# Kernel optimization log

Hardware: AMD Instinct MI355X
Metric: run time of the kernel (lower is better)

The kernel has to match this reference:

```python
import jax, jax.numpy as jnp
import numpy as np

N = 1_000_000          # number of points
V = 65536              # number of voxels / groups (static stand-in for unique(coors))
IN_CH = 64             # 3 xyz + 61 extra features
HID = 64               # feat_channels = [64, 64]
REL_HID = 16           # rel_mlp_hidden_dims = [16]
XYZ_NORM = jnp.asarray([1.0, 1.0, 1.0], dtype=jnp.float32)
REL_DIST_SCALER = jnp.float32(1.0)


def setup_inputs() -> dict:
    key = jax.random.key(0)
    ks = jax.random.split(key, 10)

    def lin(k, i, o):
        return (jax.random.normal(k, (i, o), jnp.float32) / np.sqrt(i)).astype(jnp.float32)

    return {
        "points_xyzs": jax.random.normal(ks[0], (N, 3), jnp.float32),
        "points_feat": jax.random.normal(ks[1], (N, IN_CH - 3), jnp.float32),
        "f_cluster": jax.random.normal(ks[2], (N, 3), jnp.float32),
        "coors": jax.random.randint(ks[3], (N,), 0, V, jnp.int32),
        # rel_mlp: Linear(3,16)+BN+ReLU, Linear(16,64)+BN+ReLU (inference BN folded to scale/shift)
        "rel_w0": lin(ks[4], 3, REL_HID),
        "rel_g0": jnp.ones((REL_HID,), jnp.float32),
        "rel_b0": jnp.zeros((REL_HID,), jnp.float32),
        "rel_w1": lin(ks[5], REL_HID, IN_CH),
        "rel_g1": jnp.ones((IN_CH,), jnp.float32),
        "rel_b1": jnp.zeros((IN_CH,), jnp.float32),
        # vfe layer 0: Linear(64,64)+BN+ReLU;  vfe layer 1: Linear(128,64)+BN+ReLU (in_filters*=2 for i>0)
        "vfe_w0": lin(ks[6], IN_CH, HID),
        "vfe_g0": jnp.ones((HID,), jnp.float32),
        "vfe_b0": jnp.zeros((HID,), jnp.float32),
        "vfe_w1": lin(ks[7], 2 * HID, HID),
        "vfe_g1": jnp.ones((HID,), jnp.float32),
        "vfe_b1": jnp.zeros((HID,), jnp.float32),
    }


def _bn_relu(x, g, b):
    # inference BatchNorm1d folded into per-channel scale/shift, then ReLU
    return jax.nn.relu(x * g + b)


def _forward(points_xyzs, points_feat, f_cluster, coors,
             rel_w0, rel_g0, rel_b0, rel_w1, rel_g1, rel_b1,
             vfe_w0, vfe_g0, vfe_b0, vfe_w1, vfe_g1, vfe_b1):
    xyz = points_xyzs / XYZ_NORM                              # [N, 3]
    feats = jnp.concatenate([xyz, points_feat], axis=-1)      # [N, IN_CH]
    shortcut = feats
    fc = f_cluster / REL_DIST_SCALER                          # [N, 3]
    # relative-position MLP gating: features *= rel_mlp(f_cluster)
    h = _bn_relu(fc @ rel_w0, rel_g0, rel_b0)                 # [N, REL_HID]
    gate = _bn_relu(h @ rel_w1, rel_g1, rel_b1)               # [N, IN_CH]
    feats = feats * gate
    # VFE layer 0: per-point MLP -> voxel-wise scatter max -> gather back -> concat
    p0 = _bn_relu(feats @ vfe_w0, vfe_g0, vfe_b0)             # [N, HID]
    v0 = jax.ops.segment_max(p0, coors, num_segments=V)       # [V, HID]
    v0 = jnp.where(jnp.isfinite(v0), v0, jnp.float32(0.0))    # empty voxels -> 0
    feats = jnp.concatenate([p0, v0[coors]], axis=-1)         # [N, 2*HID]
    # VFE layer 1 (last): per-point MLP, plus residual shortcut (shapes match)
    p1 = _bn_relu(feats @ vfe_w1, vfe_g1, vfe_b1)             # [N, HID]
    return p1 + shortcut


def reference(points_xyzs, points_feat, f_cluster, coors,
              rel_w0, rel_g0, rel_b0, rel_w1, rel_g1, rel_b1,
              vfe_w0, vfe_g0, vfe_b0, vfe_w1, vfe_g1, vfe_b1):
    return _forward(points_xyzs, points_feat, f_cluster, coors,
                    rel_w0, rel_g0, rel_b0, rel_w1, rel_g1, rel_b1,
                    vfe_w0, vfe_g0, vfe_b0, vfe_w1, vfe_g1, vfe_b1)
```

## Files before the change

kernel.cpp:

```cpp
#include <hip/hip_runtime.h>


#define VVOX 65536

__global__ void __launch_bounds__(256)
sir_k1a(const float* __restrict__ xyz,
        const float* __restrict__ pfeat,
        const float* __restrict__ fclu,
        const float* __restrict__ rw0,
        const float* __restrict__ rg0,
        const float* __restrict__ rb0,
        const float* __restrict__ rw1,
        const float* __restrict__ rg1,
        const float* __restrict__ rb1,
        float* __restrict__ G,
        int npts)
{
    __shared__ float s_w0[48];
    __shared__ float s_b0[16];
    __shared__ float s_w1t[1024];
    __shared__ float s_b1[64];

    const int t = threadIdx.x;
    if (t < 48) s_w0[t] = rw0[t] * rg0[t & 15];
    if (t < 16) s_b0[t] = rb0[t];
    for (int i = t; i < 1024; i += 256) {
        int k = i >> 4, j = i & 15;
        s_w1t[i] = rw1[j * 64 + k] * rg1[k];
    }
    if (t < 64) s_b1[t] = rb1[t];
    __syncthreads();

    const int pt = blockIdx.x * 256 + t;
    if (pt >= npts) return;

    const float* cr = fclu + (size_t)pt * 3;
    const float c0 = cr[0], c1 = cr[1], c2 = cr[2];
    float h[16];
    #pragma unroll
    for (int j = 0; j < 16; ++j) {
        float v = s_b0[j];
        v = fmaf(c0, s_w0[j], v);
        v = fmaf(c1, s_w0[16 + j], v);
        v = fmaf(c2, s_w0[32 + j], v);
        h[j] = fmaxf(v, 0.f);
    }

    const float* xr = xyz + (size_t)pt * 3;
    const float* fr = pfeat + (size_t)pt * 61;
    float4* Grow = reinterpret_cast<float4*>(G + (size_t)pt * 64);

    #pragma unroll 4
    for (int k4 = 0; k4 < 16; ++k4) {
        float u[4];
        #pragma unroll
        for (int kk = 0; kk < 4; ++kk) {
            const int k = k4 * 4 + kk;
            const float* w1k = s_w1t + k * 16;
            float g0 = s_b1[k], g1 = 0.f, g2 = 0.f, g3 = 0.f;
            #pragma unroll
            for (int j = 0; j < 4; ++j) {
                g0 = fmaf(h[j],      w1k[j],      g0);
                g1 = fmaf(h[4 + j],  w1k[4 + j],  g1);
                g2 = fmaf(h[8 + j],  w1k[8 + j],  g2);
                g3 = fmaf(h[12 + j], w1k[12 + j], g3);
            }
            const float g = fmaxf((g0 + g1) + (g2 + g3), 0.f);
            const float fk = (k < 3) ? xr[k] : fr[k - 3];
            u[kk] = fk * g;
        }
        float4 uu;
        uu.x = u[0]; uu.y = u[1]; uu.z = u[2]; uu.w = u[3];
        Grow[k4] = uu;
    }
}

__global__ void __launch_bounds__(256)
sir_k1b(const float* __restrict__ G,
        const int* __restrict__ coors,
        const float* __restrict__ vw0,
        const float* __restrict__ vg0,
        const float* __restrict__ vb0,
        unsigned int* __restrict__ vmax,
        float* __restrict__ p0out,
        int npts)
{
    __shared__ float s_w[4096];
    __shared__ float s_b[64];
    const int t = threadIdx.x;
    for (int i = t; i < 4096; i += 256) s_w[i] = vw0[i] * vg0[i & 63];
    if (t < 64) s_b[t] = vb0[t];
    __syncthreads();

    const int cg = t & 3;
    const int ps = t >> 2;
    const int base = blockIdx.x * 256;

    int p[4]; bool ok[4];
    const float4* Gp[4];
    #pragma unroll
    for (int i = 0; i < 4; ++i) {
        p[i] = base + ps + 64 * i;
        ok[i] = p[i] < npts;
        const int pc = ok[i] ? p[i] : 0;
        Gp[i] = reinterpret_cast<const float4*>(G + (size_t)pc * 64);
    }

    float acc[4][16];
    #pragma unroll
    for (int i = 0; i < 4; ++i)
        #pragma unroll
        for (int c = 0; c < 16; ++c) acc[i][c] = s_b[cg * 16 + c];

    float4 gv[4], gvn[4];
    #pragma unroll
    for (int i = 0; i < 4; ++i) gv[i] = Gp[i][0];

    for (int k4 = 0; k4 < 16; ++k4) {
        const int k4n = (k4 + 1) & 15;
        #pragma unroll
        for (int i = 0; i < 4; ++i) gvn[i] = Gp[i][k4n];
        const float* wb = s_w + k4 * 256 + cg * 16;
        #pragma unroll
        for (int kk = 0; kk < 4; ++kk) {
            const float* wr = wb + kk * 64;
            #pragma unroll
            for (int i = 0; i < 4; ++i) {
                const float ga[4] = { gv[i].x, gv[i].y, gv[i].z, gv[i].w };
                const float gk = ga[kk];
                #pragma unroll
                for (int c = 0; c < 16; ++c)
                    acc[i][c] = fmaf(gk, wr[c], acc[i][c]);
            }
        }
        #pragma unroll
        for (int i = 0; i < 4; ++i) gv[i] = gvn[i];
    }

    __syncthreads();

    #pragma unroll
    for (int i = 0; i < 4; ++i) {
        if (!ok[i]) continue;
        const int vox = coors[p[i]];
        unsigned int* vrow = vmax + (size_t)vox * 64 + cg * 16;
        const uint4* vrow4 = reinterpret_cast<const uint4*>(vrow);
        float4* orow = reinterpret_cast<float4*>(p0out + (size_t)p[i] * 64 + cg * 16);
        #pragma unroll
        for (int q = 0; q < 4; ++q) {
            const uint4 cur = vrow4[q];
            float4 u;
            u.x = fmaxf(acc[i][q * 4 + 0], 0.f);
            u.y = fmaxf(acc[i][q * 4 + 1], 0.f);
            u.z = fmaxf(acc[i][q * 4 + 2], 0.f);
            u.w = fmaxf(acc[i][q * 4 + 3], 0.f);
            orow[q] = u;
            if (__float_as_uint(u.x) > cur.x) atomicMax(vrow + q * 4 + 0, __float_as_uint(u.x));
            if (__float_as_uint(u.y) > cur.y) atomicMax(vrow + q * 4 + 1, __float_as_uint(u.y));
            if (__float_as_uint(u.z) > cur.z) atomicMax(vrow + q * 4 + 2, __float_as_uint(u.z));
            if (__float_as_uint(u.w) > cur.w) atomicMax(vrow + q * 4 + 3, __float_as_uint(u.w));
        }
    }
}

__global__ void __launch_bounds__(256)
sir_k2(const float* __restrict__ xyz,
       const float* __restrict__ pfeat,
       const int* __restrict__ coors,
       const float* __restrict__ vw1,
       const float* __restrict__ vg1,
       const float* __restrict__ vb1,
       const float* __restrict__ vmaxf,
       float* __restrict__ io,
       int npts)
{
    __shared__ float s_w[8192];
    __shared__ float s_b[64];
    const int t = threadIdx.x;
    for (int i = t; i < 8192; i += 256) s_w[i] = vw1[i] * vg1[i & 63];
    if (t < 64) s_b[t] = vb1[t];
    __syncthreads();

    const int cg = t & 3;
    const int ps = t >> 2;
    const int base = blockIdx.x * 256;

    int p[4]; bool ok[4];
    const float4* prow[4];
    const float4* vrow[4];
    #pragma unroll
    for (int i = 0; i < 4; ++i) {
        p[i] = base + ps + 64 * i;
        ok[i] = p[i] < npts;
        const int pc = ok[i] ? p[i] : 0;
        prow[i] = reinterpret_cast<const float4*>(io + (size_t)pc * 64);
        const int vox = coors[pc];
        vrow[i] = reinterpret_cast<const float4*>(vmaxf + (size_t)vox * 64);
    }

    float acc[4][16];
    #pragma unroll
    for (int i = 0; i < 4; ++i)
        #pragma unroll
        for (int c = 0; c < 16; ++c) acc[i][c] = s_b[cg * 16 + c];

    float4 gv[4], gvn[4];

    #pragma unroll
    for (int i = 0; i < 4; ++i) gv[i] = prow[i][0];
    for (int k4 = 0; k4 < 16; ++k4) {
        const int k4n = (k4 + 1) & 15;
        #pragma unroll
        for (int i = 0; i < 4; ++i) gvn[i] = prow[i][k4n];
        const float* wb = s_w + k4 * 256 + cg * 16;
        #pragma unroll
        for (int kk = 0; kk < 4; ++kk) {
            const float* wr = wb + kk * 64;
            #pragma unroll
            for (int i = 0; i < 4; ++i) {
                const float ga[4] = { gv[i].x, gv[i].y, gv[i].z, gv[i].w };
                const float gk = ga[kk];
                #pragma unroll
                for (int c = 0; c < 16; ++c)
                    acc[i][c] = fmaf(gk, wr[c], acc[i][c]);
            }
        }
        #pragma unroll
        for (int i = 0; i < 4; ++i) gv[i] = gvn[i];
    }

    #pragma unroll
    for (int i = 0; i < 4; ++i) gv[i] = vrow[i][0];
    for (int k4 = 0; k4 < 16; ++k4) {
        const int k4n = (k4 + 1) & 15;
        #pragma unroll
        for (int i = 0; i < 4; ++i) gvn[i] = vrow[i][k4n];
        const float* wb = s_w + 4096 + k4 * 256 + cg * 16;
        #pragma unroll
        for (int kk = 0; kk < 4; ++kk) {
            const float* wr = wb + kk * 64;
            #pragma unroll
            for (int i = 0; i < 4; ++i) {
                const float ga[4] = { gv[i].x, gv[i].y, gv[i].z, gv[i].w };
                const float gk = ga[kk];
                #pragma unroll
                for (int c = 0; c < 16; ++c)
                    acc[i][c] = fmaf(gk, wr[c], acc[i][c]);
            }
        }
        #pragma unroll
        for (int i = 0; i < 4; ++i) gv[i] = gvn[i];
    }

    __syncthreads();

    #pragma unroll
    for (int i = 0; i < 4; ++i) {
        if (!ok[i]) continue;
        const float* xr = xyz + (size_t)p[i] * 3;
        const float* fr = pfeat + (size_t)p[i] * 61;
        float4* orow = reinterpret_cast<float4*>(io + (size_t)p[i] * 64 + cg * 16);
        #pragma unroll
        for (int q = 0; q < 4; ++q) {
            const int c = cg * 16 + q * 4;
            const float s0 = (c + 0 < 3) ? xr[c + 0] : fr[c - 3];
            const float s1 = (c + 1 < 3) ? xr[c + 1] : fr[c - 2];
            const float s2 = (c + 2 < 3) ? xr[c + 2] : fr[c - 1];
            const float s3 = (c + 3 < 3) ? xr[c + 3] : fr[c + 0];
            float4 u;
            u.x = fmaxf(acc[i][q * 4 + 0], 0.f) + s0;
            u.y = fmaxf(acc[i][q * 4 + 1], 0.f) + s1;
            u.z = fmaxf(acc[i][q * 4 + 2], 0.f) + s2;
            u.w = fmaxf(acc[i][q * 4 + 3], 0.f) + s3;
            orow[q] = u;
        }
    }
}

extern "C" void kernel_launch(void* const* d_in, const int* in_sizes, int n_in,
                              void* d_out, int out_size, void* d_ws, size_t ws_size,
                              hipStream_t stream) {
    const float* xyz   = (const float*)d_in[0];
    const float* pfeat = (const float*)d_in[1];
    const float* fclu  = (const float*)d_in[2];
    const int*   coors = (const int*)d_in[3];
    const float* rw0 = (const float*)d_in[4];
    const float* rg0 = (const float*)d_in[5];
    const float* rb0 = (const float*)d_in[6];
    const float* rw1 = (const float*)d_in[7];
    const float* rg1 = (const float*)d_in[8];
    const float* rb1 = (const float*)d_in[9];
    const float* vw0 = (const float*)d_in[10];
    const float* vg0 = (const float*)d_in[11];
    const float* vb0 = (const float*)d_in[12];
    const float* vw1 = (const float*)d_in[13];
    const float* vg1 = (const float*)d_in[14];
    const float* vb1 = (const float*)d_in[15];

    float*        out  = (float*)d_out;
    unsigned int* vmax = (unsigned int*)d_ws;
    const int npts = in_sizes[3];
    const int blocks = (npts + 255) / 256;

    hipMemsetAsync(d_ws, 0, (size_t)VVOX * 64 * sizeof(float), stream);

    hipLaunchKernelGGL(sir_k1a, dim3(blocks), dim3(256), 0, stream,
                       xyz, pfeat, fclu,
                       rw0, rg0, rb0, rw1, rg1, rb1,
                       out, npts);

    hipLaunchKernelGGL(sir_k1b, dim3(blocks), dim3(256), 0, stream,
                       out, coors, vw0, vg0, vb0, vmax, out, npts);

    hipLaunchKernelGGL(sir_k2, dim3(blocks), dim3(256), 0, stream,
                       xyz, pfeat, coors,
                       vw1, vg1, vb1, (const float*)d_ws, out, npts);
}
```

Measured before the change: 1.945 ms.

## Sort points by voxel via counting sort and fuse gate MLP into VFE0

Adds a histogram, single-block scan and permutation pass that build a voxel-sorted point order. A separate pass then does the scatter-max in sorted order, and the second VFE layer also runs in sorted order, so voxel-max rows and atomics stay local. The rel-MLP gating and the first VFE matmul are fused into one per-point kernel with 64 accumulators per thread, which removes the intermediate G buffer round trip. The cost is extra sort kernels with contended atomics, a serial scan, gathered row reads of p0 in sorted order, and possibly high register pressure. An unsorted fallback is kept for when the workspace is too small.

```diff
diff --git a/kernel.cpp b/kernel.cpp
--- a/kernel.cpp
+++ b/kernel.cpp
@@ -4,22 +4,73 @@
 #define VVOX 65536
 
 __global__ void __launch_bounds__(256)
-sir_k1a(const float* __restrict__ xyz,
-        const float* __restrict__ pfeat,
-        const float* __restrict__ fclu,
-        const float* __restrict__ rw0,
-        const float* __restrict__ rg0,
-        const float* __restrict__ rb0,
-        const float* __restrict__ rw1,
-        const float* __restrict__ rg1,
-        const float* __restrict__ rb1,
-        float* __restrict__ G,
-        int npts)
+sir_hist(const int* __restrict__ coors, unsigned int* __restrict__ cnt, int npts)
+{
+    const int p = blockIdx.x * 256 + threadIdx.x;
+    if (p < npts) atomicAdd(&cnt[coors[p]], 1u);
+}
+
+__global__ void __launch_bounds__(1024)
+sir_scan(unsigned int* __restrict__ cnt)
+{
+    __shared__ unsigned int s[1024];
+    const int t = threadIdx.x;
+    unsigned int sum = 0;
+    for (int i = 0; i < 64; ++i) sum += cnt[t * 64 + i];
+    s[t] = sum;
+    __syncthreads();
+    for (int off = 1; off < 1024; off <<= 1) {
+        unsigned int v = (t >= off) ? s[t - off] : 0u;
+        __syncthreads();
+        s[t] += v;
+        __syncthreads();
+    }
+    unsigned int run = s[t] - sum;
+    for (int i = 0; i < 64; ++i) {
+        const unsigned int c = cnt[t * 64 + i];
+        cnt[t * 64 + i] = run;
+        run += c;
+    }
+}
+
+__global__ void __launch_bounds__(256)
+sir_permute(const int* __restrict__ coors, unsigned int* __restrict__ cursor,
+            unsigned int* __restrict__ perm, unsigned int* __restrict__ voxs,
+            int npts)
+{
+    const int p = blockIdx.x * 256 + threadIdx.x;
+    if (p >= npts) return;
+    const int vox = coors[p];
+    const unsigned int j = atomicAdd(&cursor[vox], 1u);
+    perm[j] = (unsigned int)p;
+    voxs[j] = (unsigned int)vox;
+}
+
+template <bool SCATTER>
+__global__ void __launch_bounds__(256)
+sir_k1(const float* __restrict__ xyz,
+       const float* __restrict__ pfeat,
+       const float* __restrict__ fclu,
+       const int* __restrict__ coors,
+       const float* __restrict__ rw0,
+       const float* __restrict__ rg0,
+       const float* __restrict__ rb0,
+       const float* __restrict__ rw1,
+       const float* __restrict__ rg1,
+       const float* __restrict__ rb1,
+       const float* __restrict__ vw0,
+       const float* __restrict__ vg0,
+       const float* __restrict__ vb0,
+       unsigned int* __restrict__ vmax,
+       float* __restrict__ p0out,
+       int npts)
 {
     __shared__ float s_w0[48];
     __shared__ float s_b0[16];
     __shared__ float s_w1t[1024];
     __shared__ float s_b1[64];
+    __shared__ float s_vw0[4096];
+    __shared__ float s_vb0[64];
 
     const int t = threadIdx.x;
     if (t < 48) s_w0[t] = rw0[t] * rg0[t & 15];
@@ -29,6 +80,8 @@
         s_w1t[i] = rw1[j * 64 + k] * rg1[k];
     }
     if (t < 64) s_b1[t] = rb1[t];
+    for (int i = t; i < 4096; i += 256) s_vw0[i] = vw0[i] * vg0[i & 63];
+    if (t < 64) s_vb0[t] = vb0[t];
     __syncthreads();
 
     const int pt = blockIdx.x * 256 + t;
@@ -46,127 +99,94 @@
         h[j] = fmaxf(v, 0.f);
     }
 
+    float acc[64];
+    #pragma unroll
+    for (int c = 0; c < 64; ++c) acc[c] = s_vb0[c];
+
     const float* xr = xyz + (size_t)pt * 3;
     const float* fr = pfeat + (size_t)pt * 61;
-    float4* Grow = reinterpret_cast<float4*>(G + (size_t)pt * 64);
-
-    #pragma unroll 4
-    for (int k4 = 0; k4 < 16; ++k4) {
-        float u[4];
-        #pragma unroll
-        for (int kk = 0; kk < 4; ++kk) {
-            const int k = k4 * 4 + kk;
-            const float* w1k = s_w1t + k * 16;
-            float g0 = s_b1[k], g1 = 0.f, g2 = 0.f, g3 = 0.f;
-            #pragma unroll
-            for (int j = 0; j < 4; ++j) {
-                g0 = fmaf(h[j],      w1k[j],      g0);
-                g1 = fmaf(h[4 + j],  w1k[4 + j],  g1);
-                g2 = fmaf(h[8 + j],  w1k[8 + j],  g2);
-                g3 = fmaf(h[12 + j], w1k[12 + j], g3);
-            }
-            const float g = fmaxf((g0 + g1) + (g2 + g3), 0.f);
-            const float fk = (k < 3) ? xr[k] : fr[k - 3];
-            u[kk] = fk * g;
-        }
-        float4 uu;
-        uu.x = u[0]; uu.y = u[1]; uu.z = u[2]; uu.w = u[3];
-        Grow[k4] = uu;
-    }
-}
-
-__global__ void __launch_bounds__(256)
-sir_k1b(const float* __restrict__ G,
-        const int* __restrict__ coors,
-        const float* __restrict__ vw0,
-        const float* __restrict__ vg0,
-        const float* __restrict__ vb0,
-        unsigned int* __restrict__ vmax,
-        float* __restrict__ p0out,
-        int npts)
-{
-    __shared__ float s_w[4096];
-    __shared__ float s_b[64];
-    const int t = threadIdx.x;
-    for (int i = t; i < 4096; i += 256) s_w[i] = vw0[i] * vg0[i & 63];
-    if (t < 64) s_b[t] = vb0[t];
-    __syncthreads();
-
-    const int cg = t & 3;
-    const int ps = t >> 2;
-    const int base = blockIdx.x * 256;
-
-    int p[4]; bool ok[4];
-    const float4* Gp[4];
-    #pragma unroll
-    for (int i = 0; i < 4; ++i) {
-        p[i] = base + ps + 64 * i;
-        ok[i] = p[i] < npts;
-        const int pc = ok[i] ? p[i] : 0;
-        Gp[i] = reinterpret_cast<const float4*>(G + (size_t)pc * 64);
-    }
-
-    float acc[4][16];
-    #pragma unroll
-    for (int i = 0; i < 4; ++i)
-        #pragma unroll
-        for (int c = 0; c < 16; ++c) acc[i][c] = s_b[cg * 16 + c];
-
-    float4 gv[4], gvn[4];
-    #pragma unroll
-    for (int i = 0; i < 4; ++i) gv[i] = Gp[i][0];
-
-    for (int k4 = 0; k4 < 16; ++k4) {
-        const int k4n = (k4 + 1) & 15;
-        #pragma unroll
-        for (int i = 0; i < 4; ++i) gvn[i] = Gp[i][k4n];
-        const float* wb = s_w + k4 * 256 + cg * 16;
-        #pragma unroll
-        for (int kk = 0; kk < 4; ++kk) {
-            const float* wr = wb + kk * 64;
-            #pragma unroll
-            for (int i = 0; i < 4; ++i) {
-                const float ga[4] = { gv[i].x, gv[i].y, gv[i].z, gv[i].w };
-                const float gk = ga[kk];
-                #pragma unroll
-                for (int c = 0; c < 16; ++c)
-                    acc[i][c] = fmaf(gk, wr[c], acc[i][c]);
-            }
-        }
-        #pragma unroll
-        for (int i = 0; i < 4; ++i) gv[i] = gvn[i];
-    }
-
-    __syncthreads();
-
-    #pragma unroll
-    for (int i = 0; i < 4; ++i) {
-        if (!ok[i]) continue;
-        const int vox = coors[p[i]];
-        unsigned int* vrow = vmax + (size_t)vox * 64 + cg * 16;
+
+    for (int k = 0; k < 64; ++k) {
+        const float* w1k = s_w1t + k * 16;
+        float g0 = s_b1[k], g1 = 0.f, g2 = 0.f, g3 = 0.f;
+        #pragma unroll
+        for (int j = 0; j < 4; ++j) {
+            g0 = fmaf(h[j],      w1k[j],      g0);
+            g1 = fmaf(h[4 + j],  w1k[4 + j],  g1);
+            g2 = fmaf(h[8 + j],  w1k[8 + j],  g2);
+            g3 = fmaf(h[12 + j], w1k[12 + j], g3);
+        }
+        const float g = fmaxf((g0 + g1) + (g2 + g3), 0.f);
+        const float fk = (k < 3) ? xr[k] : fr[k - 3];
+        const float gk = fk * g;
+        const float* wk = s_vw0 + k * 64;
+        #pragma unroll
+        for (int c = 0; c < 64; ++c) acc[c] = fmaf(gk, wk[c], acc[c]);
+    }
+
+    float4* orow = reinterpret_cast<float4*>(p0out + (size_t)pt * 64);
+    if (SCATTER) {
+        const int vox = coors[pt];
+        unsigned int* vrow = vmax + (size_t)vox * 64;
         const uint4* vrow4 = reinterpret_cast<const uint4*>(vrow);
-        float4* orow = reinterpret_cast<float4*>(p0out + (size_t)p[i] * 64 + cg * 16);
-        #pragma unroll
-        for (int q = 0; q < 4; ++q) {
+        #pragma unroll
+        for (int q = 0; q < 16; ++q) {
             const uint4 cur = vrow4[q];
             float4 u;
-            u.x = fmaxf(acc[i][q * 4 + 0], 0.f);
-            u.y = fmaxf(acc[i][q * 4 + 1], 0.f);
-            u.z = fmaxf(acc[i][q * 4 + 2], 0.f);
-            u.w = fmaxf(acc[i][q * 4 + 3], 0.f);
+            u.x = fmaxf(acc[q * 4 + 0], 0.f);
+            u.y = fmaxf(acc[q * 4 + 1], 0.f);
+            u.z = fmaxf(acc[q * 4 + 2], 0.f);
+            u.w = fmaxf(acc[q * 4 + 3], 0.f);
             orow[q] = u;
             if (__float_as_uint(u.x) > cur.x) atomicMax(vrow + q * 4 + 0, __float_as_uint(u.x));
             if (__float_as_uint(u.y) > cur.y) atomicMax(vrow + q * 4 + 1, __float_as_uint(u.y));
             if (__float_as_uint(u.z) > cur.z) atomicMax(vrow + q * 4 + 2, __float_as_uint(u.z));
             if (__float_as_uint(u.w) > cur.w) atomicMax(vrow + q * 4 + 3, __float_as_uint(u.w));
         }
-    }
-}
-
+    } else {
+        #pragma unroll
+        for (int q = 0; q < 16; ++q) {
+            float4 u;
+            u.x = fmaxf(acc[q * 4 + 0], 0.f);
+            u.y = fmaxf(acc[q * 4 + 1], 0.f);
+            u.z = fmaxf(acc[q * 4 + 2], 0.f);
+            u.w = fmaxf(acc[q * 4 + 3], 0.f);
+            orow[q] = u;
+        }
+    }
+}
+
+__global__ void __launch_bounds__(256)
+sir_kmax(const float* __restrict__ p0,
+         const unsigned int* __restrict__ perm,
+         const unsigned int* __restrict__ voxs,
+         unsigned int* __restrict__ vmax, int npts)
+{
+    const int j = blockIdx.x * 256 + threadIdx.x;
+    if (j >= npts) return;
+    const unsigned int p = perm[j];
+    const unsigned int vox = voxs[j];
+    const uint4* row = reinterpret_cast<const uint4*>(p0 + (size_t)p * 64);
+    unsigned int* vrow = vmax + (size_t)vox * 64;
+    const uint4* vrow4 = reinterpret_cast<const uint4*>(vrow);
+    #pragma unroll
+    for (int q = 0; q < 16; ++q) {
+        const uint4 pv = row[q];
+        const uint4 cur = vrow4[q];
+        if (pv.x > cur.x) atomicMax(vrow + q * 4 + 0, pv.x);
+        if (pv.y > cur.y) atomicMax(vrow + q * 4 + 1, pv.y);
+        if (pv.z > cur.z) atomicMax(vrow + q * 4 + 2, pv.z);
+        if (pv.w > cur.w) atomicMax(vrow + q * 4 + 3, pv.w);
+    }
+}
+
+template <bool SORTED>
 __global__ void __launch_bounds__(256)
 sir_k2(const float* __restrict__ xyz,
        const float* __restrict__ pfeat,
        const int* __restrict__ coors,
+       const unsigned int* __restrict__ perm,
+       const unsigned int* __restrict__ voxs,
        const float* __restrict__ vw1,
        const float* __restrict__ vg1,
        const float* __restrict__ vb1,
@@ -190,11 +210,18 @@
     const float4* vrow[4];
     #pragma unroll
     for (int i = 0; i < 4; ++i) {
-        p[i] = base + ps + 64 * i;
-        ok[i] = p[i] < npts;
-        const int pc = ok[i] ? p[i] : 0;
+        const int idx = base + ps + 64 * i;
+        ok[i] = idx < npts;
+        int pc, vox;
+        if (SORTED) {
+            pc  = ok[i] ? (int)perm[idx] : 0;
+            vox = ok[i] ? (int)voxs[idx] : 0;
+        } else {
+            pc  = ok[i] ? idx : 0;
+            vox = coors[pc];
+        }
+        p[i] = pc;
         prow[i] = reinterpret_cast<const float4*>(io + (size_t)pc * 64);
-        const int vox = coors[pc];
         vrow[i] = reinterpret_cast<const float4*>(vmaxf + (size_t)vox * 64);
     }
 
@@ -297,22 +324,44 @@
     const float* vg1 = (const float*)d_in[14];
     const float* vb1 = (const float*)d_in[15];
 
-    float*        out  = (float*)d_out;
-    unsigned int* vmax = (unsigned int*)d_ws;
+    float* out = (float*)d_out;
     const int npts = in_sizes[3];
     const int blocks = (npts + 255) / 256;
 
-    hipMemsetAsync(d_ws, 0, (size_t)VVOX * 64 * sizeof(float), stream);
-
-    hipLaunchKernelGGL(sir_k1a, dim3(blocks), dim3(256), 0, stream,
-                       xyz, pfeat, fclu,
-                       rw0, rg0, rb0, rw1, rg1, rb1,
-                       out, npts);
-
-    hipLaunchKernelGGL(sir_k1b, dim3(blocks), dim3(256), 0, stream,
-                       out, coors, vw0, vg0, vb0, vmax, out, npts);
-
-    hipLaunchKernelGGL(sir_k2, dim3(blocks), dim3(256), 0, stream,
-                       xyz, pfeat, coors,
-                       vw1, vg1, vb1, (const float*)d_ws, out, npts);
-}
+    unsigned char* ws = (unsigned char*)d_ws;
+    const size_t VMAX_B = (size_t)VVOX * 64 * sizeof(unsigned int);
+    unsigned int* vmax = (unsigned int*)ws;
+    unsigned int* cnt  = (unsigned int*)(ws + VMAX_B);
+    unsigned int* perm = (unsigned int*)(ws + VMAX_B + (size_t)VVOX * 4);
+    unsigned int* voxs = perm + npts;
+    const size_t needed = VMAX_B + (size_t)VVOX * 4 + 2 * (size_t)npts * 4;
+
+    hipMemsetAsync(vmax, 0, VMAX_B, stream);
+
+    if (ws_size >= needed) {
+        hipMemsetAsync(cnt, 0, (size_t)VVOX * 4, stream);
+        hipLaunchKernelGGL(sir_hist, dim3(blocks), dim3(256), 0, stream,
+                           coors, cnt, npts);
+        hipLaunchKernelGGL(sir_scan, dim3(1), dim3(1024), 0, stream, cnt);
+        hipLaunchKernelGGL(sir_permute, dim3(blocks), dim3(256), 0, stream,
+                           coors, cnt, perm, voxs, npts);
+        hipLaunchKernelGGL(HIP_KERNEL_NAME(sir_k1<false>), dim3(blocks), dim3(256), 0, stream,
+                           xyz, pfeat, fclu, coors,
+                           rw0, rg0, rb0, rw1, rg1, rb1,
+                           vw0, vg0, vb0, vmax, out, npts);
+        hipLaunchKernelGGL(sir_kmax, dim3(blocks), dim3(256), 0, stream,
+                           out, perm, voxs, vmax, npts);
+        hipLaunchKernelGGL(HIP_KERNEL_NAME(sir_k2<true>), dim3(blocks), dim3(256), 0, stream,
+                           xyz, pfeat, coors, perm, voxs,
+                           vw1, vg1, vb1, (const float*)vmax, out, npts);
+    } else {
+        hipLaunchKernelGGL(HIP_KERNEL_NAME(sir_k1<true>), dim3(blocks), dim3(256), 0, stream,
+                           xyz, pfeat, fclu, coors,
+                           rw0, rg0, rb0, rw1, rg1, rb1,
+                           vw0, vg0, vb0, vmax, out, npts);
+        hipLaunchKernelGGL(HIP_KERNEL_NAME(sir_k2<false>), dim3(blocks), dim3(256), 0, stream,
+                           xyz, pfeat, coors, (const unsigned int*)nullptr,
+                           (const unsigned int*)nullptr,
+                           vw1, vg1, vb1, (const float*)vmax, out, npts);
+    }
+}
```

Result: slower. 2.634 ms (+35.4%).
